# Optimization experiments

Measured on AMD Instinct MI355X. Metric: run time of the kernel, lower is better.

## Reference

```python
import jax, jax.numpy as jnp
from jax import lax
import numpy as np

# Geometry fixed by __init__ (see shape_source)
UP = 2          # up_factor[0]
DOWN = 2        # down_factor[0]
PAD_LO = 11
PAD_HI = 10
SLOPE = 0.2
GAIN = np.sqrt(2.0).astype(np.float32)


def _kaiser_beta(atten):
    if atten > 50:
        return 0.1102 * (atten - 8.7)
    if atten > 21:
        return 0.5842 * (atten - 21.0) ** 0.4 + 0.07886 * (atten - 21.0)
    return 0.0


def _firwin(numtaps, cutoff, width, fs):
    # numpy re-implementation of scipy.signal.firwin(numtaps, cutoff, width=width, fs=fs)
    nyq = fs / 2.0
    atten = 2.285 * (numtaps - 1) * np.pi * (width / nyq) + 7.95  # kaiser_atten
    beta = _kaiser_beta(atten)
    m = np.arange(numtaps) - (numtaps - 1) / 2.0
    fc = cutoff / nyq
    h = fc * np.sinc(fc * m) * np.kaiser(numtaps, beta)
    h = h / h.sum()  # unity DC gain (pass_zero scaling)
    return h.astype(np.float32)


def _depthwise_conv1d(x, f, axis, stride=1, lhs_dilation=1, padding=(0, 0)):
    """Depthwise 1D FIR along spatial `axis` (2 or 3) of NCHW tensor.
    Filter is flipped (true convolution, as in upfirdn2d)."""
    C = x.shape[1]
    k = f.shape[0]
    fr = f[::-1]
    if axis == 2:
        kern = jnp.broadcast_to(fr.reshape(1, 1, k, 1), (C, 1, k, 1))
        strides, ld, pads = (stride, 1), (lhs_dilation, 1), [padding, (0, 0)]
    else:
        kern = jnp.broadcast_to(fr.reshape(1, 1, 1, k), (C, 1, 1, k))
        strides, ld, pads = (1, stride), (1, lhs_dilation), [(0, 0), padding]
    return lax.conv_general_dilated(
        x, kern, window_strides=strides, padding=pads, lhs_dilation=ld,
        dimension_numbers=('NCHW', 'OIHW', 'NCHW'), feature_group_count=C)


def setup_inputs() -> dict:
    key = jax.random.key(0)
    k1, k2 = jax.random.split(key)
    x = jax.random.normal(k1, (32, 128, 64, 64), dtype=jnp.float32)
    bias = jax.random.normal(k2, (128,), dtype=jnp.float32) * 0.1
    # up filter: numtaps=12, cutoff=in_cutoff=28, width=2*in_half_width=8, fs=tmp_sr=128
    up_filter = jnp.asarray(_firwin(12, 28.0, 8.0, 128.0))
    # down filter: numtaps=12, cutoff=out_cutoff=28, width=2*out_half_width=8, fs=128
    down_filter = jnp.asarray(_firwin(12, 28.0, 8.0, 128.0))
    return {"x": x, "bias": bias, "up_filter": up_filter, "down_filter": down_filter}


def reference(x, bias, up_filter, down_filter):
    # filtered_lrelu reference: upfirdn2d(up, fu, gain=up**2) -> bias -> lrelu*sqrt(2) -> upfirdn2d(down, fd)
    # Zero-insertion upsampling fused via lhs_dilation; dilated length is H*UP-(UP-1),
    # so the trailing UP-1 zeros of the nominal H*UP upsampled signal move into pad_hi.
    fu = up_filter * UP  # gain up per separable pass -> up**2 total
    pad = (PAD_LO, PAD_HI + UP - 1)
    y = _depthwise_conv1d(x, fu, axis=2, lhs_dilation=UP, padding=pad)
    y = _depthwise_conv1d(y, fu, axis=3, lhs_dilation=UP, padding=pad)  # [B,C,138,138]
    y = y + bias[None, :, None, None]
    y = jnp.where(y >= 0, y, SLOPE * y) * GAIN
    y = _depthwise_conv1d(y, down_filter, axis=2, stride=DOWN)
    y = _depthwise_conv1d(y, down_filter, axis=3, stride=DOWN)  # [B,C,64,64]
    return y
```

## Files before the change

### kernel.cpp

```cpp
#include <hip/hip_runtime.h>


#define NT 1024
#define SLOPE 0.2f
#define GAIN 1.41421356237309504880f

#define ZROWS 74
#define ZSTRIDE 84
#define ZPAD 8
#define YROWS 74
#define YSTRIDE 148
#define YWSTRIDE 68

#define ZB_OFF 0
#define YB_OFF (ZROWS * ZSTRIDE)
#define YW_OFF 0
#define LDS_FLOATS (YB_OFF + YROWS * YSTRIDE)

__global__ __launch_bounds__(NT, 8) void fused_upfirdn_lrelu(
    const float* __restrict__ x,
    const float* __restrict__ bias,
    const float* __restrict__ upf,
    const float* __restrict__ dnf,
    float* __restrict__ out)
{
    extern __shared__ float lds[];
    float* zb = lds + ZB_OFF;
    float* yb = lds + YB_OFF;
    float* yw = lds + YW_OFF;

    const int t = threadIdx.x;
    const int bid = blockIdx.x;
    const int s = bid >> 1;
    const int o0 = (bid & 1) << 5;
    const int c = s & 127;

    float fu[12], fd[12];
#pragma unroll
    for (int j = 0; j < 12; ++j) { fu[j] = 2.0f * upf[j]; fd[j] = dnf[j]; }
    const float bv = bias[c];

    const float* xg = x + (size_t)s * 4096;
    float* outg = out + (size_t)s * 4096;

    if (t < 304) {
        const int k = t >> 4;
        const int c4 = (t & 15) << 2;
        const int rbase = o0 - 5 + 2 * k;
        float4 xv[7];
#pragma unroll
        for (int d = 0; d < 7; ++d) {
            const int r = rbase + d;
            if (r >= 0 && r <= 63)
                xv[d] = *reinterpret_cast<const float4*>(xg + r * 64 + c4);
            else
                xv[d] = make_float4(0.f, 0.f, 0.f, 0.f);
        }
        float a0[4] = {0,0,0,0}, a1[4] = {0,0,0,0}, b0[4] = {0,0,0,0}, b1[4] = {0,0,0,0};
#pragma unroll
        for (int d = 0; d < 6; ++d) {
            const float w0 = fu[2 * (5 - d)], w1 = fu[2 * (5 - d) + 1];
            a0[0] += w0 * xv[d].x; a0[1] += w0 * xv[d].y; a0[2] += w0 * xv[d].z; a0[3] += w0 * xv[d].w;
            a1[0] += w1 * xv[d].x; a1[1] += w1 * xv[d].y; a1[2] += w1 * xv[d].z; a1[3] += w1 * xv[d].w;
        }
#pragma unroll
        for (int d = 1; d < 7; ++d) {
            const float w0 = fu[2 * (6 - d)], w1 = fu[2 * (6 - d) + 1];
            b0[0] += w0 * xv[d].x; b0[1] += w0 * xv[d].y; b0[2] += w0 * xv[d].z; b0[3] += w0 * xv[d].w;
            b1[0] += w1 * xv[d].x; b1[1] += w1 * xv[d].y; b1[2] += w1 * xv[d].z; b1[3] += w1 * xv[d].w;
        }
        float* zr = zb + (4 * k) * ZSTRIDE + ZPAD + c4;
        *reinterpret_cast<float4*>(zr)               = make_float4(a0[0], a0[1], a0[2], a0[3]);
        *reinterpret_cast<float4*>(zr + ZSTRIDE)     = make_float4(a1[0], a1[1], a1[2], a1[3]);
        if (k < 18) {
            *reinterpret_cast<float4*>(zr + 2 * ZSTRIDE) = make_float4(b0[0], b0[1], b0[2], b0[3]);
            *reinterpret_cast<float4*>(zr + 3 * ZSTRIDE) = make_float4(b1[0], b1[1], b1[2], b1[3]);
        }
    } else if (t < 674) {
        const int pt = t - 304;
        const int rl = pt / 5;
        const int p = pt - rl * 5;
        const int col = (p < 2) ? (p << 2) : (72 + ((p - 2) << 2));
        *reinterpret_cast<float4*>(zb + rl * ZSTRIDE + col) = make_float4(0.f, 0.f, 0.f, 0.f);
    }
    __syncthreads();

    if (t < 720) {
        const int m8 = t / 80;
        const int il = t - m8 * 80;
        if (il < YROWS) {
            const int mbase = m8 << 3;
            const float* zr = zb + il * ZSTRIDE + mbase;
            float zv[16];
#pragma unroll
            for (int q = 0; q < 4; ++q) {
                const float4 v = *reinterpret_cast<const float4*>(zr + (q << 2));
                zv[4 * q] = v.x; zv[4 * q + 1] = v.y; zv[4 * q + 2] = v.z; zv[4 * q + 3] = v.w;
            }
            float yv[16];
#pragma unroll
            for (int e = 0; e < 8; ++e) {
                float a0 = 0.0f, a1 = 0.0f;
#pragma unroll
                for (int tt = 0; tt < 6; ++tt) {
                    const float zz = zv[8 + e - tt];
                    a0 += fu[2 * tt]     * zz;
                    a1 += fu[2 * tt + 1] * zz;
                }
                a0 += bv; a1 += bv;
                a0 = (a0 >= 0.0f ? a0 : SLOPE * a0) * GAIN;
                a1 = (a1 >= 0.0f ? a1 : SLOPE * a1) * GAIN;
                yv[2 * e] = a0; yv[2 * e + 1] = a1;
            }
            float* yr = yb + il * YSTRIDE + (mbase << 1);
#pragma unroll
            for (int q = 0; q < 4; ++q)
                *reinterpret_cast<float4*>(yr + (q << 2)) =
                    make_float4(yv[4 * q], yv[4 * q + 1], yv[4 * q + 2], yv[4 * q + 3]);
        }
    }
    __syncthreads();

    if (t < 640) {
        const int cg = t / 80;
        const int il = t - cg * 80;
        if (il < YROWS) {
            const float* yr = yb + il * YSTRIDE + (cg << 4);
            float w[28];
#pragma unroll
            for (int q = 0; q < 7; ++q) {
                const float4 v = *reinterpret_cast<const float4*>(yr + (q << 2));
                w[4 * q] = v.x; w[4 * q + 1] = v.y; w[4 * q + 2] = v.z; w[4 * q + 3] = v.w;
            }
            float rv[8];
#pragma unroll
            for (int e = 0; e < 8; ++e) {
                float a = 0.0f;
#pragma unroll
                for (int j = 0; j < 12; ++j) a += fd[j] * w[2 * e + 11 - j];
                rv[e] = a;
            }
            float* wr = yw + il * YWSTRIDE + (cg << 3);
            *reinterpret_cast<float4*>(wr)     = make_float4(rv[0], rv[1], rv[2], rv[3]);
            *reinterpret_cast<float4*>(wr + 4) = make_float4(rv[4], rv[5], rv[6], rv[7]);
        }
    }
    __syncthreads();

    if (t < 128) {
        const int eg = t >> 4;
        const int col4 = (t & 15) << 2;
        const float* wr = yw + (eg << 3) * YWSTRIDE + col4;
        float acc[4][4] = {{0,0,0,0},{0,0,0,0},{0,0,0,0},{0,0,0,0}};
#pragma unroll
        for (int r = 0; r < 18; ++r) {
            const float4 v = *reinterpret_cast<const float4*>(wr + r * YWSTRIDE);
#pragma unroll
            for (int e = 0; e < 4; ++e) {
                if (r >= 2 * e && r <= 2 * e + 11) {
                    const float ww = fd[11 - r + 2 * e];
                    acc[e][0] += ww * v.x; acc[e][1] += ww * v.y;
                    acc[e][2] += ww * v.z; acc[e][3] += ww * v.w;
                }
            }
        }
#pragma unroll
        for (int e = 0; e < 4; ++e)
            *reinterpret_cast<float4*>(outg + (o0 + (eg << 2) + e) * 64 + col4) =
                make_float4(acc[e][0], acc[e][1], acc[e][2], acc[e][3]);
    }
}

extern "C" void kernel_launch(void* const* d_in, const int* in_sizes, int n_in,
                              void* d_out, int out_size, void* d_ws, size_t ws_size,
                              hipStream_t stream) {
    const float* x    = (const float*)d_in[0];
    const float* bias = (const float*)d_in[1];
    const float* upf  = (const float*)d_in[2];
    const float* dnf  = (const float*)d_in[3];
    float* out = (float*)d_out;

    const int n_blocks = 32 * 128 * 2;
    const size_t lds_bytes = (size_t)LDS_FLOATS * sizeof(float);
    hipLaunchKernelGGL(fused_upfirdn_lrelu, dim3(n_blocks), dim3(NT),
                       lds_bytes, stream, x, bias, upf, dnf, out);
}
```

Before: 73.72 us.

## Fuse horizontal upsample, lrelu and horizontal downsample into one stage

Merges the horizontal up-FIR plus bias/lrelu stage with the horizontal down-FIR stage, so each thread keeps the upsampled row segment in registers instead of staging it in a large LDS buffer. This drops one barrier and the intermediate yb buffer, which shrinks LDS per block and lets the block size fall from 1024 to 640 threads. Leaky ReLU with gain is rewritten branch-free as C1*a + C2*|a|. In exchange, neighbouring threads recompute overlapping upsampled values (13 pairs per thread to produce 8 outputs), and register pressure rises.

```diff
diff --git a/kernel.cpp b/kernel.cpp
--- a/kernel.cpp
+++ b/kernel.cpp
@@ -1,21 +1,19 @@
 #include <hip/hip_runtime.h>
 
 
-#define NT 1024
-#define SLOPE 0.2f
+#define NT 640
 #define GAIN 1.41421356237309504880f
+#define C1 (0.6f * GAIN)
+#define C2 (0.4f * GAIN)
 
 #define ZROWS 74
 #define ZSTRIDE 84
 #define ZPAD 8
-#define YROWS 74
-#define YSTRIDE 148
 #define YWSTRIDE 68
 
 #define ZB_OFF 0
-#define YB_OFF (ZROWS * ZSTRIDE)
-#define YW_OFF 0
-#define LDS_FLOATS (YB_OFF + YROWS * YSTRIDE)
+#define YW_OFF (ZROWS * ZSTRIDE)
+#define LDS_FLOATS (YW_OFF + ZROWS * YWSTRIDE)
 
 __global__ __launch_bounds__(NT, 8) void fused_upfirdn_lrelu(
     const float* __restrict__ x,
@@ -26,7 +24,6 @@
 {
     extern __shared__ float lds[];
     float* zb = lds + ZB_OFF;
-    float* yb = lds + YB_OFF;
     float* yw = lds + YW_OFF;
 
     const int t = threadIdx.x;
@@ -76,73 +73,51 @@
             *reinterpret_cast<float4*>(zr + 2 * ZSTRIDE) = make_float4(b0[0], b0[1], b0[2], b0[3]);
             *reinterpret_cast<float4*>(zr + 3 * ZSTRIDE) = make_float4(b1[0], b1[1], b1[2], b1[3]);
         }
-    } else if (t < 674) {
-        const int pt = t - 304;
-        const int rl = pt / 5;
-        const int p = pt - rl * 5;
-        const int col = (p < 2) ? (p << 2) : (72 + ((p - 2) << 2));
-        *reinterpret_cast<float4*>(zb + rl * ZSTRIDE + col) = make_float4(0.f, 0.f, 0.f, 0.f);
-    }
-    __syncthreads();
-
-    if (t < 720) {
-        const int m8 = t / 80;
-        const int il = t - m8 * 80;
-        if (il < YROWS) {
-            const int mbase = m8 << 3;
-            const float* zr = zb + il * ZSTRIDE + mbase;
-            float zv[16];
-#pragma unroll
-            for (int q = 0; q < 4; ++q) {
-                const float4 v = *reinterpret_cast<const float4*>(zr + (q << 2));
-                zv[4 * q] = v.x; zv[4 * q + 1] = v.y; zv[4 * q + 2] = v.z; zv[4 * q + 3] = v.w;
-            }
-            float yv[16];
-#pragma unroll
-            for (int e = 0; e < 8; ++e) {
-                float a0 = 0.0f, a1 = 0.0f;
-#pragma unroll
-                for (int tt = 0; tt < 6; ++tt) {
-                    const float zz = zv[8 + e - tt];
-                    a0 += fu[2 * tt]     * zz;
-                    a1 += fu[2 * tt + 1] * zz;
-                }
-                a0 += bv; a1 += bv;
-                a0 = (a0 >= 0.0f ? a0 : SLOPE * a0) * GAIN;
-                a1 = (a1 >= 0.0f ? a1 : SLOPE * a1) * GAIN;
-                yv[2 * e] = a0; yv[2 * e + 1] = a1;
-            }
-            float* yr = yb + il * YSTRIDE + (mbase << 1);
-#pragma unroll
-            for (int q = 0; q < 4; ++q)
-                *reinterpret_cast<float4*>(yr + (q << 2)) =
-                    make_float4(yv[4 * q], yv[4 * q + 1], yv[4 * q + 2], yv[4 * q + 3]);
+    } else {
+        for (int pt = t - 304; pt < 370; pt += 336) {
+            const int rl = pt / 5;
+            const int p = pt - rl * 5;
+            const int col = (p < 2) ? (p << 2) : (72 + ((p - 2) << 2));
+            *reinterpret_cast<float4*>(zb + rl * ZSTRIDE + col) = make_float4(0.f, 0.f, 0.f, 0.f);
         }
     }
     __syncthreads();
 
-    if (t < 640) {
+    {
         const int cg = t / 80;
         const int il = t - cg * 80;
-        if (il < YROWS) {
-            const float* yr = yb + il * YSTRIDE + (cg << 4);
-            float w[28];
+        if (il < ZROWS) {
+            const float* zr = zb + il * ZSTRIDE + (cg << 3);
+            float zv[24];
 #pragma unroll
-            for (int q = 0; q < 7; ++q) {
-                const float4 v = *reinterpret_cast<const float4*>(yr + (q << 2));
-                w[4 * q] = v.x; w[4 * q + 1] = v.y; w[4 * q + 2] = v.z; w[4 * q + 3] = v.w;
+            for (int q = 0; q < 6; ++q) {
+                const float4 v = *reinterpret_cast<const float4*>(zr + (q << 2));
+                zv[4 * q] = v.x; zv[4 * q + 1] = v.y; zv[4 * q + 2] = v.z; zv[4 * q + 3] = v.w;
             }
-            float rv[8];
+            float yv[26];
+#pragma unroll
+            for (int v = 0; v < 13; ++v) {
+                float a0 = bv, a1 = bv;
+#pragma unroll
+                for (int tt = 0; tt < 6; ++tt) {
+                    const float zz = zv[v + 8 - tt];
+                    a0 += fu[2 * tt]     * zz;
+                    a1 += fu[2 * tt + 1] * zz;
+                }
+                yv[2 * v]     = C1 * a0 + C2 * fabsf(a0);
+                yv[2 * v + 1] = C1 * a1 + C2 * fabsf(a1);
+            }
+            float acc[8];
 #pragma unroll
             for (int e = 0; e < 8; ++e) {
                 float a = 0.0f;
 #pragma unroll
-                for (int j = 0; j < 12; ++j) a += fd[j] * w[2 * e + 11 - j];
-                rv[e] = a;
+                for (int j = 0; j < 12; ++j) a += fd[j] * yv[2 * e + 11 - j];
+                acc[e] = a;
             }
             float* wr = yw + il * YWSTRIDE + (cg << 3);
-            *reinterpret_cast<float4*>(wr)     = make_float4(rv[0], rv[1], rv[2], rv[3]);
-            *reinterpret_cast<float4*>(wr + 4) = make_float4(rv[4], rv[5], rv[6], rv[7]);
+            *reinterpret_cast<float4*>(wr)     = make_float4(acc[0], acc[1], acc[2], acc[3]);
+            *reinterpret_cast<float4*>(wr + 4) = make_float4(acc[4], acc[5], acc[6], acc[7]);
         }
     }
     __syncthreads();
```

Result: slower. 105.5 us (+43.0%).

## Split each plane into four 16-row tiles with 512-thread blocks

Applied to the files above, without the earlier changes.

Each block now produces 16 output rows instead of 32, so twice as many blocks run with 512 threads each and a smaller LDS footprint (42 intermediate rows). This shrinks per-block LDS and work so more blocks can be resident at once, at the cost of more halo recompute and redundant input loads across tiles. Filter taps and bias are also forced into scalar registers via readfirstlane, and the leaky ReLU is rewritten branch-free as a linear term plus an abs term.

```diff
diff --git a/kernel.cpp b/kernel.cpp
--- a/kernel.cpp
+++ b/kernel.cpp
@@ -1,21 +1,25 @@
 #include <hip/hip_runtime.h>
 
 
-#define NT 1024
-#define SLOPE 0.2f
+#define NT 512
 #define GAIN 1.41421356237309504880f
+#define C1 (0.6f * GAIN)
+#define C2 (0.4f * GAIN)
 
-#define ZROWS 74
+#define ZROWS 42
 #define ZSTRIDE 84
 #define ZPAD 8
-#define YROWS 74
 #define YSTRIDE 148
 #define YWSTRIDE 68
 
 #define ZB_OFF 0
 #define YB_OFF (ZROWS * ZSTRIDE)
 #define YW_OFF 0
-#define LDS_FLOATS (YB_OFF + YROWS * YSTRIDE)
+#define LDS_FLOATS (YB_OFF + ZROWS * YSTRIDE)
+
+__device__ __forceinline__ float sload(float v) {
+    return __uint_as_float(__builtin_amdgcn_readfirstlane(__float_as_uint(v)));
+}
 
 __global__ __launch_bounds__(NT, 8) void fused_upfirdn_lrelu(
     const float* __restrict__ x,
@@ -31,143 +35,128 @@
 
     const int t = threadIdx.x;
     const int bid = blockIdx.x;
-    const int s = bid >> 1;
-    const int o0 = (bid & 1) << 5;
+    const int s = bid >> 2;
+    const int o0 = (bid & 3) << 4;
     const int c = s & 127;
 
     float fu[12], fd[12];
 #pragma unroll
-    for (int j = 0; j < 12; ++j) { fu[j] = 2.0f * upf[j]; fd[j] = dnf[j]; }
-    const float bv = bias[c];
+    for (int j = 0; j < 12; ++j) {
+        fu[j] = sload(2.0f * upf[j]);
+        fd[j] = sload(dnf[j]);
+    }
+    const float bv = sload(bias[c]);
 
     const float* xg = x + (size_t)s * 4096;
     float* outg = out + (size_t)s * 4096;
 
-    if (t < 304) {
-        const int k = t >> 4;
+    if (t < 336) {
+        const int m = t >> 4;
         const int c4 = (t & 15) << 2;
-        const int rbase = o0 - 5 + 2 * k;
-        float4 xv[7];
+        const int M = o0 + m;
+        float4 xv[6];
+        if (M >= 5 && M <= 63) {
 #pragma unroll
-        for (int d = 0; d < 7; ++d) {
-            const int r = rbase + d;
-            if (r >= 0 && r <= 63)
-                xv[d] = *reinterpret_cast<const float4*>(xg + r * 64 + c4);
-            else
-                xv[d] = make_float4(0.f, 0.f, 0.f, 0.f);
+            for (int d = 0; d < 6; ++d)
+                xv[d] = *reinterpret_cast<const float4*>(xg + (M - 5 + d) * 64 + c4);
+        } else {
+#pragma unroll
+            for (int d = 0; d < 6; ++d) {
+                const int r = M - 5 + d;
+                xv[d] = (r >= 0 && r <= 63)
+                      ? *reinterpret_cast<const float4*>(xg + r * 64 + c4)
+                      : make_float4(0.f, 0.f, 0.f, 0.f);
+            }
         }
-        float a0[4] = {0,0,0,0}, a1[4] = {0,0,0,0}, b0[4] = {0,0,0,0}, b1[4] = {0,0,0,0};
+        float a0[4] = {0,0,0,0}, a1[4] = {0,0,0,0};
 #pragma unroll
         for (int d = 0; d < 6; ++d) {
             const float w0 = fu[2 * (5 - d)], w1 = fu[2 * (5 - d) + 1];
             a0[0] += w0 * xv[d].x; a0[1] += w0 * xv[d].y; a0[2] += w0 * xv[d].z; a0[3] += w0 * xv[d].w;
             a1[0] += w1 * xv[d].x; a1[1] += w1 * xv[d].y; a1[2] += w1 * xv[d].z; a1[3] += w1 * xv[d].w;
         }
-#pragma unroll
-        for (int d = 1; d < 7; ++d) {
-            const float w0 = fu[2 * (6 - d)], w1 = fu[2 * (6 - d) + 1];
-            b0[0] += w0 * xv[d].x; b0[1] += w0 * xv[d].y; b0[2] += w0 * xv[d].z; b0[3] += w0 * xv[d].w;
-            b1[0] += w1 * xv[d].x; b1[1] += w1 * xv[d].y; b1[2] += w1 * xv[d].z; b1[3] += w1 * xv[d].w;
-        }
-        float* zr = zb + (4 * k) * ZSTRIDE + ZPAD + c4;
-        *reinterpret_cast<float4*>(zr)               = make_float4(a0[0], a0[1], a0[2], a0[3]);
-        *reinterpret_cast<float4*>(zr + ZSTRIDE)     = make_float4(a1[0], a1[1], a1[2], a1[3]);
-        if (k < 18) {
-            *reinterpret_cast<float4*>(zr + 2 * ZSTRIDE) = make_float4(b0[0], b0[1], b0[2], b0[3]);
-            *reinterpret_cast<float4*>(zr + 3 * ZSTRIDE) = make_float4(b1[0], b1[1], b1[2], b1[3]);
-        }
-    } else if (t < 674) {
-        const int pt = t - 304;
-        const int rl = pt / 5;
-        const int p = pt - rl * 5;
-        const int col = (p < 2) ? (p << 2) : (72 + ((p - 2) << 2));
-        *reinterpret_cast<float4*>(zb + rl * ZSTRIDE + col) = make_float4(0.f, 0.f, 0.f, 0.f);
-    }
-    __syncthreads();
-
-    if (t < 720) {
-        const int m8 = t / 80;
-        const int il = t - m8 * 80;
-        if (il < YROWS) {
-            const int mbase = m8 << 3;
-            const float* zr = zb + il * ZSTRIDE + mbase;
-            float zv[16];
-#pragma unroll
-            for (int q = 0; q < 4; ++q) {
-                const float4 v = *reinterpret_cast<const float4*>(zr + (q << 2));
-                zv[4 * q] = v.x; zv[4 * q + 1] = v.y; zv[4 * q + 2] = v.z; zv[4 * q + 3] = v.w;
-            }
-            float yv[16];
-#pragma unroll
-            for (int e = 0; e < 8; ++e) {
-                float a0 = 0.0f, a1 = 0.0f;
-#pragma unroll
-                for (int tt = 0; tt < 6; ++tt) {
-                    const float zz = zv[8 + e - tt];
-                    a0 += fu[2 * tt]     * zz;
-                    a1 += fu[2 * tt + 1] * zz;
-                }
-                a0 += bv; a1 += bv;
-                a0 = (a0 >= 0.0f ? a0 : SLOPE * a0) * GAIN;
-                a1 = (a1 >= 0.0f ? a1 : SLOPE * a1) * GAIN;
-                yv[2 * e] = a0; yv[2 * e + 1] = a1;
-            }
-            float* yr = yb + il * YSTRIDE + (mbase << 1);
-#pragma unroll
-            for (int q = 0; q < 4; ++q)
-                *reinterpret_cast<float4*>(yr + (q << 2)) =
-                    make_float4(yv[4 * q], yv[4 * q + 1], yv[4 * q + 2], yv[4 * q + 3]);
+        float* zr = zb + (2 * m) * ZSTRIDE + ZPAD + c4;
+        *reinterpret_cast<float4*>(zr)           = make_float4(a0[0], a0[1], a0[2], a0[3]);
+        *reinterpret_cast<float4*>(zr + ZSTRIDE) = make_float4(a1[0], a1[1], a1[2], a1[3]);
+    } else {
+        for (int pt = t - 336; pt < 210; pt += 176) {
+            const int rl = pt / 5;
+            const int p = pt - rl * 5;
+            const int col = (p < 2) ? (p << 2) : (72 + ((p - 2) << 2));
+            *reinterpret_cast<float4*>(zb + rl * ZSTRIDE + col) = make_float4(0.f, 0.f, 0.f, 0.f);
         }
     }
     __syncthreads();
 
-    if (t < 640) {
-        const int cg = t / 80;
-        const int il = t - cg * 80;
-        if (il < YROWS) {
-            const float* yr = yb + il * YSTRIDE + (cg << 4);
-            float w[28];
+    if (t < 378) {
+        const int cg = t / 42;
+        const int il = t - cg * 42;
+        const int mbase = cg << 3;
+        const float* zr = zb + il * ZSTRIDE + mbase;
+        float zv[16];
 #pragma unroll
-            for (int q = 0; q < 7; ++q) {
-                const float4 v = *reinterpret_cast<const float4*>(yr + (q << 2));
-                w[4 * q] = v.x; w[4 * q + 1] = v.y; w[4 * q + 2] = v.z; w[4 * q + 3] = v.w;
+        for (int q = 0; q < 4; ++q) {
+            const float4 v = *reinterpret_cast<const float4*>(zr + (q << 2));
+            zv[4 * q] = v.x; zv[4 * q + 1] = v.y; zv[4 * q + 2] = v.z; zv[4 * q + 3] = v.w;
+        }
+        float yv[16];
+#pragma unroll
+        for (int e = 0; e < 8; ++e) {
+            float a0 = bv, a1 = bv;
+#pragma unroll
+            for (int tt = 0; tt < 6; ++tt) {
+                const float zz = zv[8 + e - tt];
+                a0 += fu[2 * tt]     * zz;
+                a1 += fu[2 * tt + 1] * zz;
             }
-            float rv[8];
+            yv[2 * e]     = C1 * a0 + C2 * fabsf(a0);
+            yv[2 * e + 1] = C1 * a1 + C2 * fabsf(a1);
+        }
+        float* yr = yb + il * YSTRIDE + (mbase << 1);
 #pragma unroll
-            for (int e = 0; e < 8; ++e) {
-                float a = 0.0f;
-#pragma unroll
-                for (int j = 0; j < 12; ++j) a += fd[j] * w[2 * e + 11 - j];
-                rv[e] = a;
-            }
-            float* wr = yw + il * YWSTRIDE + (cg << 3);
-            *reinterpret_cast<float4*>(wr)     = make_float4(rv[0], rv[1], rv[2], rv[3]);
-            *reinterpret_cast<float4*>(wr + 4) = make_float4(rv[4], rv[5], rv[6], rv[7]);
-        }
+        for (int q = 0; q < 4; ++q)
+            *reinterpret_cast<float4*>(yr + (q << 2)) =
+                make_float4(yv[4 * q], yv[4 * q + 1], yv[4 * q + 2], yv[4 * q + 3]);
     }
     __syncthreads();
 
-    if (t < 128) {
-        const int eg = t >> 4;
+    if (t < 336) {
+        const int cg = t / 42;
+        const int il = t - cg * 42;
+        const float* yr = yb + il * YSTRIDE + (cg << 4);
+        float w[28];
+#pragma unroll
+        for (int q = 0; q < 7; ++q) {
+            const float4 v = *reinterpret_cast<const float4*>(yr + (q << 2));
+            w[4 * q] = v.x; w[4 * q + 1] = v.y; w[4 * q + 2] = v.z; w[4 * q + 3] = v.w;
+        }
+        float rv[8];
+#pragma unroll
+        for (int e = 0; e < 8; ++e) {
+            float a = 0.0f;
+#pragma unroll
+            for (int j = 0; j < 12; ++j) a += fd[j] * w[2 * e + 11 - j];
+            rv[e] = a;
+        }
+        float* wr = yw + il * YWSTRIDE + (cg << 3);
+        *reinterpret_cast<float4*>(wr)     = make_float4(rv[0], rv[1], rv[2], rv[3]);
+        *reinterpret_cast<float4*>(wr + 4) = make_float4(rv[4], rv[5], rv[6], rv[7]);
+    }
+    __syncthreads();
+
+    if (t < 256) {
+        const int o = t >> 4;
         const int col4 = (t & 15) << 2;
-        const float* wr = yw + (eg << 3) * YWSTRIDE + col4;
-        float acc[4][4] = {{0,0,0,0},{0,0,0,0},{0,0,0,0},{0,0,0,0}};
+        const float* wr = yw + (2 * o) * YWSTRIDE + col4;
+        float a0 = 0.f, a1 = 0.f, a2 = 0.f, a3 = 0.f;
 #pragma unroll
-        for (int r = 0; r < 18; ++r) {
-            const float4 v = *reinterpret_cast<const float4*>(wr + r * YWSTRIDE);
-#pragma unroll
-            for (int e = 0; e < 4; ++e) {
-                if (r >= 2 * e && r <= 2 * e + 11) {
-                    const float ww = fd[11 - r + 2 * e];
-                    acc[e][0] += ww * v.x; acc[e][1] += ww * v.y;
-                    acc[e][2] += ww * v.z; acc[e][3] += ww * v.w;
-                }
-            }
+        for (int rr = 0; rr < 12; ++rr) {
+            const float4 v = *reinterpret_cast<const float4*>(wr + rr * YWSTRIDE);
+            const float ww = fd[11 - rr];
+            a0 += ww * v.x; a1 += ww * v.y; a2 += ww * v.z; a3 += ww * v.w;
         }
-#pragma unroll
-        for (int e = 0; e < 4; ++e)
-            *reinterpret_cast<float4*>(outg + (o0 + (eg << 2) + e) * 64 + col4) =
-                make_float4(acc[e][0], acc[e][1], acc[e][2], acc[e][3]);
+        *reinterpret_cast<float4*>(outg + (o0 + o) * 64 + col4) =
+            make_float4(a0, a1, a2, a3);
     }
 }
 
@@ -180,7 +169,7 @@
     const float* dnf  = (const float*)d_in[3];
     float* out = (float*)d_out;
 
-    const int n_blocks = 32 * 128 * 2;
+    const int n_blocks = 32 * 128 * 4;
     const size_t lds_bytes = (size_t)LDS_FLOATS * sizeof(float);
     hipLaunchKernelGGL(fused_upfirdn_lrelu, dim3(n_blocks), dim3(NT),
                        lds_bytes, stream, x, bias, upf, dnf, out);
```

Result: no change. 73.24 us (-0.7%).
